# Kernel optimization log

Hardware: AMD Instinct MI355X
Metric: run time of the kernel (lower is better)

Reference implementation:

```python
import jax, jax.numpy as jnp
import numpy as np

D_MODEL = 512
NUM_HEADS = 8


def setup_inputs() -> dict:
    key = jax.random.key(0)
    ks = jax.random.split(key, 6)
    B, T, D = 4, 2048, D_MODEL
    x = jax.random.normal(ks[0], (B, T, D), dtype=jnp.float32)
    periods = jax.random.randint(ks[1], (B, NUM_HEADS), 0, 48)
    # nn.MultiheadAttention parameters: packed qkv in-projection + out-projection
    in_proj_w = jax.random.normal(ks[2], (3 * D, D), dtype=jnp.float32) * 0.02
    in_proj_b = jax.random.normal(ks[3], (3 * D,), dtype=jnp.float32) * 0.02
    out_w = jax.random.normal(ks[4], (D, D), dtype=jnp.float32) * 0.02
    out_b = jax.random.normal(ks[5], (D,), dtype=jnp.float32) * 0.02
    return {"x": x, "periods": periods, "in_proj_w": in_proj_w,
            "in_proj_b": in_proj_b, "out_w": out_w, "out_b": out_b}


def reference(x, periods, in_proj_w, in_proj_b, out_w, out_b):
    B, T, D = x.shape
    H = periods.shape[1]          # one head per period (num_heads == top_k)
    hd = D // H
    # packed qkv projection (matches torch in_proj_weight layout)
    qkv = x @ in_proj_w.T + in_proj_b            # (B,T,3D)
    q, k, v = jnp.split(qkv, 3, axis=-1)
    def to_heads(t):
        return t.reshape(B, T, H, hd).transpose(0, 2, 1, 3)  # (B,H,T,hd)
    q, k, v = to_heads(q), to_heads(k), to_heads(v)
    scores = jnp.einsum('bhqd,bhkd->bhqk', q, k) / jnp.sqrt(jnp.asarray(hd, x.dtype))
    # periodic causal mask: allow j<=i with (i-j) % P == 0
    i = jnp.arange(T)[:, None]
    j = jnp.arange(T)[None, :]
    p = jnp.maximum(periods, 1)[:, :, None, None]            # (B,H,1,1)
    allow = (j <= i) & (((i - j) % p) == 0)                  # (B,H,T,T)
    scores = jnp.where(allow, scores, -jnp.inf)              # diagonal always allowed -> no all-masked rows
    attn = jax.nn.softmax(scores, axis=-1)
    out = jnp.einsum('bhqk,bhkd->bhqd', attn, v)             # (B,H,T,hd)
    out = out.transpose(0, 2, 1, 3).reshape(B, T, D)
    return out @ out_w.T + out_b
```

## Files before the change

kernel.cpp:

```cpp
#include <hip/hip_runtime.h>
#include <math.h>

#define D_MODEL 512
#define NHEAD   8
#define HD      64
#define T_SEQ   2048
#define BATCH   4
#define M_ROWS  (BATCH * T_SEQ)

typedef __attribute__((ext_vector_type(8))) short  short8;
typedef __attribute__((ext_vector_type(4))) float  floatx4;

__device__ __forceinline__ unsigned short f2bf(float f) {
    unsigned int u = __float_as_uint(f);
    unsigned int r = u + 0x7FFFu + ((u >> 16) & 1u);
    return (unsigned short)(r >> 16);
}

__device__ __forceinline__ float bf2f(unsigned short u) {
    return __uint_as_float((unsigned int)u << 16);
}

__device__ __forceinline__ int4 cvt8(float4 a, float4 b) {
    union { unsigned short u[8]; int4 v; } r;
    r.u[0] = f2bf(a.x); r.u[1] = f2bf(a.y); r.u[2] = f2bf(a.z); r.u[3] = f2bf(a.w);
    r.u[4] = f2bf(b.x); r.u[5] = f2bf(b.y); r.u[6] = f2bf(b.z); r.u[7] = f2bf(b.w);
    return r.v;
}

__device__ __forceinline__ bool slot_decode(int t, int P, int& r, int& mt, int& Lr)
{
    const int q0 = T_SEQ / P, rem = T_SEQ % P;
    const int nt_hi = (q0 + 64) >> 6;
    const int nt_lo = (q0 + 63) >> 6;
    const int hi_total = rem * nt_hi;
    if (t < hi_total) {
        r = t / nt_hi; mt = t - r * nt_hi; Lr = q0 + 1;
    } else {
        t -= hi_total;
        if (t >= (P - rem) * nt_lo) return false;
        const int rr = t / nt_lo;
        r = rem + rr; mt = t - rr * nt_lo; Lr = q0;
    }
    return true;
}

__global__ __launch_bounds__(256) void qkv_gemm_mfma(
    const float* __restrict__ X,
    const float* __restrict__ W,
    const float* __restrict__ bias,
    unsigned short* __restrict__ qo, unsigned short* __restrict__ ko,
    unsigned short* __restrict__ vo)
{
    __shared__ unsigned short smem[128 * 128];
    unsigned short* const As = smem;
    unsigned short* const Bs = smem + 128 * 64;

    const int bid  = blockIdx.x;
    const int xcd  = bid & 7;
    const int chk_ = bid >> 3;
    const int row0 = (((chk_ / 12) << 3) + xcd) << 7;
    const int col0 = (chk_ % 12) << 7;

    const int tid  = threadIdx.x;
    const int wave = tid >> 6, lane = tid & 63;
    const int quad = lane >> 4, l15 = lane & 15;
    const int wm   = wave >> 1, wn = wave & 1;
    const int lr8  = lane >> 3;
    const int sc   = lane & 7;

    floatx4 acc[4][4] = {};

    for (int k0 = 0; k0 < D_MODEL; k0 += 64) {
        int4 av[4], bv[4];
#pragma unroll
        for (int i = 0; i < 4; ++i) {
            const int r = wave * 32 + i * 8 + lr8;
            const float* ap = X + (size_t)(row0 + r) * D_MODEL + k0 + (sc << 3);
            const float* bp = W + (size_t)(col0 + r) * D_MODEL + k0 + (sc << 3);
            av[i] = cvt8(*(const float4*)ap, *(const float4*)(ap + 4));
            bv[i] = cvt8(*(const float4*)bp, *(const float4*)(bp + 4));
        }
        __syncthreads();
#pragma unroll
        for (int i = 0; i < 4; ++i) {
            const int r  = wave * 32 + i * 8 + lr8;
            const int cp = (sc ^ (r & 7)) << 3;
            *(int4*)(As + (r << 6) + cp) = av[i];
            *(int4*)(Bs + (r << 6) + cp) = bv[i];
        }
        __syncthreads();

#pragma unroll
        for (int ks = 0; ks < 2; ++ks) {
            short8 af[4], bfr[4];
            const int ch = (ks << 2) + quad;
#pragma unroll
            for (int mt = 0; mt < 4; ++mt) {
                const int row = (wm << 6) + (mt << 4) + l15;
                af[mt] = *(const short8*)(As + (row << 6) + ((ch ^ (row & 7)) << 3));
            }
#pragma unroll
            for (int nt = 0; nt < 4; ++nt) {
                const int col = (wn << 6) + (nt << 4) + l15;
                bfr[nt] = *(const short8*)(Bs + (col << 6) + ((ch ^ (col & 7)) << 3));
            }
#pragma unroll
            for (int mt = 0; mt < 4; ++mt)
#pragma unroll
                for (int nt = 0; nt < 4; ++nt)
                    acc[mt][nt] = __builtin_amdgcn_mfma_f32_16x16x32_bf16(
                        af[mt], bfr[nt], acc[mt][nt], 0, 0, 0);
        }
    }

    __syncthreads();
#pragma unroll
    for (int nt = 0; nt < 4; ++nt) {
        const int ncol = (wn << 6) + (nt << 4) + l15;
        const float bn = bias[col0 + ncol];
#pragma unroll
        for (int mt = 0; mt < 4; ++mt)
#pragma unroll
            for (int reg = 0; reg < 4; ++reg) {
                const int mrow = (wm << 6) + (mt << 4) + (quad << 2) + reg;
                smem[(mrow << 7) + ncol] = f2bf(acc[mt][nt][reg] + bn);
            }
    }
    __syncthreads();
    {
        const int c16  = lane & 15;
        const int rsub = lane >> 4;
        const int n0   = col0 + (c16 << 3);
        const int part = n0 >> 9;
        unsigned short* dst = (part == 0) ? qo : ((part == 1) ? ko : vo);
        const int head = (n0 & 511) >> 6, d0 = n0 & 63;
#pragma unroll
        for (int p = 0; p < 8; ++p) {
            const int ml = (wave << 5) + (p << 2) + rsub;
            const int m  = row0 + ml;
            const int b = m >> 11, t = m & 2047;
            int4 val = *(const int4*)(smem + (ml << 7) + (c16 << 3));
            *(int4*)(dst + ((((size_t)b << 3) + head) * T_SEQ + t) * HD + d0) = val;
        }
    }
}

__global__ __launch_bounds__(256) void attn_rc_mfma(
    const unsigned short* __restrict__ q, const unsigned short* __restrict__ k,
    const unsigned short* __restrict__ v, const int* __restrict__ periods,
    unsigned short* __restrict__ o,
    unsigned short* __restrict__ Opart, float* __restrict__ Mpart,
    float* __restrict__ Lpart)
{
    __shared__ unsigned short Ks[2][64 * 64];
    __shared__ unsigned short Vt[2][64 * 64];
    __shared__ unsigned short Ps[64 * 64];

    const int bh = blockIdx.y;
    int P = periods[bh]; if (P < 1) P = 1;
    const int t_orig = blockIdx.x;
    const int c = blockIdx.z;
    int r, mt, Lr;
    if (!slot_decode(t_orig, P, r, mt, Lr)) return;
    if ((c << 3) > mt) return;
    const int nch  = (mt >> 3) + 1;
    const int kt0  = c << 3;
    const int kend = (kt0 + 7 < mt) ? (kt0 + 7) : mt;
    const int m0 = mt << 6;

    const int tid  = threadIdx.x;
    const int wave = tid >> 6, lane = tid & 63;
    const int quad = lane >> 4, l15 = lane & 15;
    const int srow = tid >> 2;
    const int vkp  = tid & 31, vhg = tid >> 5;

    const unsigned short* hq = q + (size_t)bh * T_SEQ * HD;
    const unsigned short* hk = k + (size_t)bh * T_SEQ * HD;
    const unsigned short* hv = v + (size_t)bh * T_SEQ * HD;

    const short8 vone = {16256, 16256, 16256, 16256,
                         16256, 16256, 16256, 16256};

    {
        int m = m0 + srow; if (m > Lr - 1) m = Lr - 1;
        const unsigned short* src = hq + (size_t)(r + m * P) * HD;
#pragma unroll
        for (int rep = 0; rep < 2; ++rep) {
            const int cc = ((tid & 3) << 1) + rep;
            int4 a = *(const int4*)(src + (cc << 3));
            *(int4*)(Ps + (srow << 6) + ((cc ^ (srow & 7)) << 3)) = a;
        }
    }
    {
        const int km0 = kt0 << 6;
        int mk = km0 + srow; if (mk > Lr - 1) mk = Lr - 1;
        const unsigned short* ksrc = hk + (size_t)(r + mk * P) * HD;
#pragma unroll
        for (int rep = 0; rep < 2; ++rep) {
            const int cc = ((tid & 3) << 1) + rep;
            int4 a = *(const int4*)(ksrc + (cc << 3));
            *(int4*)(Ks[0] + (srow << 6) + ((cc ^ (srow & 7)) << 3)) = a;
        }
        int mv0 = km0 + (vkp << 1);     if (mv0 > Lr - 1) mv0 = Lr - 1;
        int mv1 = km0 + (vkp << 1) + 1; if (mv1 > Lr - 1) mv1 = Lr - 1;
        int4 va = *(const int4*)(hv + (size_t)(r + mv0 * P) * HD + (vhg << 3));
        int4 vb = *(const int4*)(hv + (size_t)(r + mv1 * P) * HD + (vhg << 3));
        const unsigned short* pa = (const unsigned short*)&va;
        const unsigned short* pb = (const unsigned short*)&vb;
#pragma unroll
        for (int j = 0; j < 8; ++j) {
            const int hd_ = (vhg << 3) + j;
            const unsigned int pk =
                (unsigned int)pa[j] | ((unsigned int)pb[j] << 16);
            *(unsigned int*)((char*)Vt[0] + (hd_ << 7) +
                             ((((vkp >> 2) ^ (hd_ & 7)) << 4)) +
                             ((vkp & 3) << 2)) = pk;
        }
    }
    __syncthreads();
    short8 qf[2];
#pragma unroll
    for (int ks = 0; ks < 2; ++ks) {
        const int row = (wave << 4) + l15;
        qf[ks] = *(const short8*)(Ps + (row << 6) +
                                  ((((ks << 2) + quad) ^ (row & 7)) << 3));
    }

    floatx4 Oa[4] = {};
    float m_i[4] = {-1e30f, -1e30f, -1e30f, -1e30f};
    float l_i[4] = {0.f, 0.f, 0.f, 0.f};

    for (int kt = kt0; kt <= kend; ++kt) {
        const int buf = (kt - kt0) & 1;
        const bool havenext = kt < kend;

        int4 ka[2], va, vb;
        if (havenext) {
            const int km0 = (kt + 1) << 6;
            int mk = km0 + srow; if (mk > Lr - 1) mk = Lr - 1;
            const unsigned short* ksrc = hk + (size_t)(r + mk * P) * HD;
#pragma unroll
            for (int rep = 0; rep < 2; ++rep)
                ka[rep] = *(const int4*)(ksrc + ((((tid & 3) << 1) + rep) << 3));
            int mv0 = km0 + (vkp << 1);     if (mv0 > Lr - 1) mv0 = Lr - 1;
            int mv1 = km0 + (vkp << 1) + 1; if (mv1 > Lr - 1) mv1 = Lr - 1;
            va = *(const int4*)(hv + (size_t)(r + mv0 * P) * HD + (vhg << 3));
            vb = *(const int4*)(hv + (size_t)(r + mv1 * P) * HD + (vhg << 3));
        }

        floatx4 sacc[4] = {};
#pragma unroll
        for (int nt = 0; nt < 4; ++nt) {
            const int row = (nt << 4) + l15;
#pragma unroll
            for (int ks = 0; ks < 2; ++ks) {
                short8 kf = *(const short8*)(Ks[buf] + (row << 6) +
                                             ((((ks << 2) + quad) ^ (row & 7)) << 3));
                sacc[nt] = __builtin_amdgcn_mfma_f32_16x16x32_bf16(
                    qf[ks], kf, sacc[nt], 0, 0, 0);
            }
        }

        const bool diag = (kt == mt);
        float s[4][4];
        float tm = -1e30f;
#pragma unroll
        for (int nt = 0; nt < 4; ++nt)
#pragma unroll
            for (int reg = 0; reg < 4; ++reg) {
                float sv = sacc[nt][reg] * 0.125f;
                if (diag) {
                    const int sq = (wave << 4) + (quad << 2) + reg;
                    if (((nt << 4) + l15) > sq) sv = -1e30f;
                }
                s[nt][reg] = sv;
                tm = fmaxf(tm, sv);
            }
        tm = fmaxf(tm, __shfl_xor(tm, 1));
        tm = fmaxf(tm, __shfl_xor(tm, 2));
        tm = fmaxf(tm, __shfl_xor(tm, 4));
        tm = fmaxf(tm, __shfl_xor(tm, 8));
        tm = fmaxf(tm, __shfl_xor(tm, 16));
        tm = fmaxf(tm, __shfl_xor(tm, 32));

        float sc[4];
#pragma unroll
        for (int reg = 0; reg < 4; ++reg) {
            const float nm = fmaxf(m_i[reg], tm);
            sc[reg] = __expf(m_i[reg] - nm);
            m_i[reg] = nm;
        }

#pragma unroll
        for (int reg = 0; reg < 4; ++reg) {
            const int row = (wave << 4) + (quad << 2) + reg;
#pragma unroll
            for (int nt = 0; nt < 4; ++nt) {
                const int col = (nt << 4) + l15;
                *((unsigned short*)((char*)Ps + (row << 7) +
                                    (((col >> 3) ^ (row & 7)) << 4) +
                                    ((col & 7) << 1))) =
                    f2bf(__expf(s[nt][reg] - m_i[reg]));
            }
        }

        short8 pf[2];
#pragma unroll
        for (int ks = 0; ks < 2; ++ks) {
            const int row = (wave << 4) + l15;
            pf[ks] = *(const short8*)(Ps + (row << 6) +
                                      ((((ks << 2) + quad) ^ (row & 7)) << 3));
        }
        floatx4 ls = {};
        ls = __builtin_amdgcn_mfma_f32_16x16x32_bf16(pf[0], vone, ls, 0, 0, 0);
        ls = __builtin_amdgcn_mfma_f32_16x16x32_bf16(pf[1], vone, ls, 0, 0, 0);
#pragma unroll
        for (int reg = 0; reg < 4; ++reg)
            l_i[reg] = l_i[reg] * sc[reg] + ls[reg];

#pragma unroll
        for (int nt = 0; nt < 4; ++nt)
#pragma unroll
            for (int reg = 0; reg < 4; ++reg)
                Oa[nt][reg] *= sc[reg];
#pragma unroll
        for (int nt = 0; nt < 4; ++nt) {
            const int row = (nt << 4) + l15;
#pragma unroll
            for (int ks = 0; ks < 2; ++ks) {
                short8 vf = *(const short8*)(Vt[buf] + (row << 6) +
                                             ((((ks << 2) + quad) ^ (row & 7)) << 3));
                Oa[nt] = __builtin_amdgcn_mfma_f32_16x16x32_bf16(
                    pf[ks], vf, Oa[nt], 0, 0, 0);
            }
        }

        if (havenext) {
#pragma unroll
            for (int rep = 0; rep < 2; ++rep) {
                const int cc = ((tid & 3) << 1) + rep;
                *(int4*)(Ks[buf ^ 1] + (srow << 6) + ((cc ^ (srow & 7)) << 3)) = ka[rep];
            }
            const unsigned short* pa = (const unsigned short*)&va;
            const unsigned short* pb = (const unsigned short*)&vb;
#pragma unroll
            for (int j = 0; j < 8; ++j) {
                const int hd_ = (vhg << 3) + j;
                const unsigned int pk =
                    (unsigned int)pa[j] | ((unsigned int)pb[j] << 16);
                *(unsigned int*)((char*)Vt[buf ^ 1] + (hd_ << 7) +
                                 ((((vkp >> 2) ^ (hd_ & 7)) << 4)) +
                                 ((vkp & 3) << 2)) = pk;
            }
        }
        __syncthreads();
    }

    if (nch == 1) {
#pragma unroll
        for (int reg = 0; reg < 4; ++reg) {
            const float invl = 1.f / l_i[reg];
            const int row = (wave << 4) + (quad << 2) + reg;
#pragma unroll
            for (int nt = 0; nt < 4; ++nt)
                Ks[0][(row << 6) + (nt << 4) + l15] = f2bf(Oa[nt][reg] * invl);
        }
        const int lrow = lane >> 2;
        const int chk  = (lane & 3) << 1;
        const int ml   = (wave << 4) + lrow;
        const int m    = m0 + ml;
        if (m < Lr) {
            const size_t base = ((size_t)bh * T_SEQ + (r + m * P)) * HD;
            int4 w0 = *(const int4*)(Ks[0] + (ml << 6) + (chk << 3));
            int4 w1 = *(const int4*)(Ks[0] + (ml << 6) + ((chk + 1) << 3));
            *(int4*)(o + base + (chk << 3))       = w0;
            *(int4*)(o + base + ((chk + 1) << 3)) = w1;
        }
    } else {
        const size_t slot = ((size_t)((bh << 6) + t_orig) << 2) + c;
#pragma unroll
        for (int reg = 0; reg < 4; ++reg) {
            const int row = (wave << 4) + (quad << 2) + reg;
#pragma unroll
            for (int nt = 0; nt < 4; ++nt)
                Ks[0][(row << 6) + (nt << 4) + l15] = f2bf(Oa[nt][reg]);
            if (l15 == 0) {
                Mpart[slot * 64 + row] = m_i[reg];
                Lpart[slot * 64 + row] = l_i[reg];
            }
        }
        const int lrow = lane >> 2;
        const int chk  = (lane & 3) << 1;
        const int ml   = (wave << 4) + lrow;
        unsigned short* dst = Opart + slot * 4096 + (ml << 6);
        *(int4*)(dst + (chk << 3))       = *(const int4*)(Ks[0] + (ml << 6) + (chk << 3));
        *(int4*)(dst + ((chk + 1) << 3)) = *(const int4*)(Ks[0] + (ml << 6) + ((chk + 1) << 3));
    }
}

__global__ __launch_bounds__(256) void reduce_rc(
    const int* __restrict__ periods,
    const unsigned short* __restrict__ Opart, const float* __restrict__ Mpart,
    const float* __restrict__ Lpart, unsigned short* __restrict__ o)
{
    const int bh = blockIdx.y;
    int P = periods[bh]; if (P < 1) P = 1;
    const int t = blockIdx.x;
    int r, mt, Lr;
    if (!slot_decode(t, P, r, mt, Lr)) return;
    const int nch = (mt >> 3) + 1;
    if (nch < 2) return;

    const int tid = threadIdx.x;
    const int row = tid >> 2;
    const int cg  = (tid & 3) << 4;
    const int m   = (mt << 6) + row;
    if (m >= Lr) return;

    const size_t slot0 = (size_t)((bh << 6) + t) << 2;

    float mv[4], lv[4];
    float mm = -1e30f;
    for (int cc = 0; cc < nch; ++cc) {
        mv[cc] = Mpart[(slot0 + cc) * 64 + row];
        lv[cc] = Lpart[(slot0 + cc) * 64 + row];
        mm = fmaxf(mm, mv[cc]);
    }
    float lsum = 0.f, a[4];
    for (int cc = 0; cc < nch; ++cc) {
        a[cc] = __expf(mv[cc] - mm);
        lsum += a[cc] * lv[cc];
    }
    const float inv = 1.f / lsum;

    float ov[16] = {};
    for (int cc = 0; cc < nch; ++cc) {
        const unsigned short* p = Opart + (slot0 + cc) * 4096 + (row << 6) + cg;
        const float ac = a[cc];
#pragma unroll
        for (int j = 0; j < 16; ++j) ov[j] += ac * bf2f(p[j]);
    }
    unsigned short outv[16];
#pragma unroll
    for (int j = 0; j < 16; ++j) outv[j] = f2bf(ov[j] * inv);

    unsigned short* dst = o + ((size_t)bh * T_SEQ + (r + m * P)) * HD + cg;
    *(int4*)dst       = *(const int4*)&outv[0];
    *(int4*)(dst + 8) = *(const int4*)&outv[8];
}

__global__ __launch_bounds__(256) void out_gemm_mfma(
    const unsigned short* __restrict__ A,
    const float* __restrict__ W,
    const float* __restrict__ bias,
    float* __restrict__ out)
{
    __shared__ unsigned short As[128 * 64];
    __shared__ unsigned short Bs[128 * 64];

    const int tid  = threadIdx.x;
    const int wave = tid >> 6, lane = tid & 63;
    const int quad = lane >> 4, l15 = lane & 15;
    const int wm   = wave >> 1, wn = wave & 1;
    const int row0 = blockIdx.x * 128;
    const int col0 = blockIdx.y * 128;
    const int lr8  = lane >> 3;
    const int sc   = lane & 7;

    floatx4 acc[4][4] = {};

    for (int k0 = 0; k0 < D_MODEL; k0 += 64) {
        const int h = k0 >> 6;
        int4 av[4], bv[4];
#pragma unroll
        for (int i = 0; i < 4; ++i) {
            const int r  = wave * 32 + i * 8 + lr8;
            const int rg = row0 + r;
            const int b = rg >> 11, t = rg & 2047;
            av[i] = *(const int4*)(A + ((((size_t)b << 3) + h) * T_SEQ + t) * HD + (sc << 3));
            const float* bp = W + (size_t)(col0 + r) * D_MODEL + k0 + (sc << 3);
            bv[i] = cvt8(*(const float4*)bp, *(const float4*)(bp + 4));
        }
        __syncthreads();
#pragma unroll
        for (int i = 0; i < 4; ++i) {
            const int r  = wave * 32 + i * 8 + lr8;
            const int cp = (sc ^ (r & 7)) << 3;
            *(int4*)(As + (r << 6) + cp) = av[i];
            *(int4*)(Bs + (r << 6) + cp) = bv[i];
        }
        __syncthreads();

#pragma unroll
        for (int ks = 0; ks < 2; ++ks) {
            short8 af[4], bfr[4];
            const int ch = (ks << 2) + quad;
#pragma unroll
            for (int mt = 0; mt < 4; ++mt) {
                const int row = (wm << 6) + (mt << 4) + l15;
                af[mt] = *(const short8*)(As + (row << 6) + ((ch ^ (row & 7)) << 3));
            }
#pragma unroll
            for (int nt = 0; nt < 4; ++nt) {
                const int col = (wn << 6) + (nt << 4) + l15;
                bfr[nt] = *(const short8*)(Bs + (col << 6) + ((ch ^ (col & 7)) << 3));
            }
#pragma unroll
            for (int mt = 0; mt < 4; ++mt)
#pragma unroll
                for (int nt = 0; nt < 4; ++nt)
                    acc[mt][nt] = __builtin_amdgcn_mfma_f32_16x16x32_bf16(
                        af[mt], bfr[nt], acc[mt][nt], 0, 0, 0);
        }
    }

#pragma unroll
    for (int nt = 0; nt < 4; ++nt) {
        const int n = col0 + (wn << 6) + (nt << 4) + l15;
        const float bn = bias[n];
#pragma unroll
        for (int mt = 0; mt < 4; ++mt) {
#pragma unroll
            for (int reg = 0; reg < 4; ++reg) {
                const int m = row0 + (wm << 6) + (mt << 4) + (quad << 2) + reg;
                out[(size_t)m * D_MODEL + n] = acc[mt][nt][reg] + bn;
            }
        }
    }
}

extern "C" void kernel_launch(void* const* d_in, const int* in_sizes, int n_in,
                              void* d_out, int out_size, void* d_ws, size_t ws_size,
                              hipStream_t stream)
{
    const float* x        = (const float*)d_in[0];
    const int*   periods  = (const int*)  d_in[1];
    const float* in_w     = (const float*)d_in[2];
    const float* in_b     = (const float*)d_in[3];
    const float* out_w    = (const float*)d_in[4];
    const float* out_b    = (const float*)d_in[5];
    float*       out      = (float*)d_out;

    const size_t TENS = (size_t)BATCH * NHEAD * T_SEQ * HD;
    unsigned short* qb    = (unsigned short*)d_ws;
    unsigned short* kb    = qb + TENS;
    unsigned short* vb    = kb + TENS;
    unsigned short* aob   = vb + TENS;
    unsigned short* Opart = aob + TENS;
    float*          Mpart = (float*)(Opart + (size_t)8192 * 4096);
    float*          Lpart = Mpart + (size_t)8192 * 64;

    qkv_gemm_mfma<<<(M_ROWS / 128) * ((3 * D_MODEL) / 128), 256, 0, stream>>>(
        x, in_w, in_b, qb, kb, vb);

    dim3 g2(64, BATCH * NHEAD, 4);
    attn_rc_mfma<<<g2, 256, 0, stream>>>(qb, kb, vb, periods, aob,
                                         Opart, Mpart, Lpart);
    reduce_rc<<<dim3(64, BATCH * NHEAD), 256, 0, stream>>>(
        periods, Opart, Mpart, Lpart, aob);

    dim3 g3(M_ROWS / 128, D_MODEL / 128);
    out_gemm_mfma<<<g3, 256, 0, stream>>>(aob, out_w, out_b, out);
}
```

Baseline: 166.2 us.

## Pre-convert inputs to bf16 and stage GEMM tiles via direct global-to-LDS loads

Adds a conversion kernel that turns x and both weight matrices into bf16 buffers in workspace once per call. The QKV and output GEMMs then load these bf16 tiles straight into LDS with global_load_lds, using a swizzled source address instead of register staging, and add a barrier at the end of each k-step. The aim is to halve GEMM load bytes, stop each tile from re-converting the same weights, and skip the register round trip. The cost is an extra launch plus a full write and read of the bf16 copies.

```diff
diff --git a/kernel.cpp b/kernel.cpp
--- a/kernel.cpp
+++ b/kernel.cpp
@@ -26,6 +26,12 @@
     r.u[0] = f2bf(a.x); r.u[1] = f2bf(a.y); r.u[2] = f2bf(a.z); r.u[3] = f2bf(a.w);
     r.u[4] = f2bf(b.x); r.u[5] = f2bf(b.y); r.u[6] = f2bf(b.z); r.u[7] = f2bf(b.w);
     return r.v;
+}
+
+__device__ __forceinline__ void gload16(const void* g, void* l) {
+    __builtin_amdgcn_global_load_lds(
+        (const __attribute__((address_space(1))) void*)g,
+        (__attribute__((address_space(3))) void*)l, 16, 0, 0);
 }
 
 __device__ __forceinline__ bool slot_decode(int t, int P, int& r, int& mt, int& Lr)
@@ -45,9 +51,29 @@
     return true;
 }
 
+#define XGROUPS  (M_ROWS * D_MODEL / 8)
+#define W1GROUPS (3 * D_MODEL * D_MODEL / 8)
+#define W2GROUPS (D_MODEL * D_MODEL / 8)
+#define CVT_GROUPS (XGROUPS + W1GROUPS + W2GROUPS)
+
+__global__ __launch_bounds__(256) void cvt_inputs(
+    const float* __restrict__ x, const float* __restrict__ w1,
+    const float* __restrict__ w2, unsigned short* __restrict__ xo,
+    unsigned short* __restrict__ w1o, unsigned short* __restrict__ w2o)
+{
+    int i = blockIdx.x * 256 + threadIdx.x;
+    const float* src; unsigned short* dst;
+    if (i < XGROUPS)                  { src = x;  dst = xo;  }
+    else if (i < XGROUPS + W1GROUPS)  { src = w1; dst = w1o; i -= XGROUPS; }
+    else                              { src = w2; dst = w2o; i -= XGROUPS + W1GROUPS; }
+    const float4* p = (const float4*)(src + (size_t)i * 8);
+    float4 a = p[0], b = p[1];
+    *(int4*)(dst + (size_t)i * 8) = cvt8(a, b);
+}
+
 __global__ __launch_bounds__(256) void qkv_gemm_mfma(
-    const float* __restrict__ X,
-    const float* __restrict__ W,
+    const unsigned short* __restrict__ X,
+    const unsigned short* __restrict__ W,
     const float* __restrict__ bias,
     unsigned short* __restrict__ qo, unsigned short* __restrict__ ko,
     unsigned short* __restrict__ vo)
@@ -72,22 +98,15 @@
     floatx4 acc[4][4] = {};
 
     for (int k0 = 0; k0 < D_MODEL; k0 += 64) {
-        int4 av[4], bv[4];
 #pragma unroll
         for (int i = 0; i < 4; ++i) {
-            const int r = wave * 32 + i * 8 + lr8;
-            const float* ap = X + (size_t)(row0 + r) * D_MODEL + k0 + (sc << 3);
-            const float* bp = W + (size_t)(col0 + r) * D_MODEL + k0 + (sc << 3);
-            av[i] = cvt8(*(const float4*)ap, *(const float4*)(ap + 4));
-            bv[i] = cvt8(*(const float4*)bp, *(const float4*)(bp + 4));
-        }
-        __syncthreads();
-#pragma unroll
-        for (int i = 0; i < 4; ++i) {
-            const int r  = wave * 32 + i * 8 + lr8;
-            const int cp = (sc ^ (r & 7)) << 3;
-            *(int4*)(As + (r << 6) + cp) = av[i];
-            *(int4*)(Bs + (r << 6) + cp) = bv[i];
+            const int rb  = (wave << 5) + (i << 3);
+            const int r   = rb + lr8;
+            const int csw = sc ^ (r & 7);
+            gload16(X + (size_t)(row0 + r) * D_MODEL + k0 + (csw << 3),
+                    As + (rb << 6));
+            gload16(W + (size_t)(col0 + r) * D_MODEL + k0 + (csw << 3),
+                    Bs + (rb << 6));
         }
         __syncthreads();
 
@@ -112,9 +131,9 @@
                     acc[mt][nt] = __builtin_amdgcn_mfma_f32_16x16x32_bf16(
                         af[mt], bfr[nt], acc[mt][nt], 0, 0, 0);
         }
-    }
-
-    __syncthreads();
+        __syncthreads();
+    }
+
 #pragma unroll
     for (int nt = 0; nt < 4; ++nt) {
         const int ncol = (wn << 6) + (nt << 4) + l15;
@@ -452,7 +471,7 @@
 
 __global__ __launch_bounds__(256) void out_gemm_mfma(
     const unsigned short* __restrict__ A,
-    const float* __restrict__ W,
+    const unsigned short* __restrict__ W,
     const float* __restrict__ bias,
     float* __restrict__ out)
 {
@@ -472,23 +491,17 @@
 
     for (int k0 = 0; k0 < D_MODEL; k0 += 64) {
         const int h = k0 >> 6;
-        int4 av[4], bv[4];
 #pragma unroll
         for (int i = 0; i < 4; ++i) {
-            const int r  = wave * 32 + i * 8 + lr8;
+            const int rb  = (wave << 5) + (i << 3);
+            const int r   = rb + lr8;
+            const int csw = sc ^ (r & 7);
             const int rg = row0 + r;
             const int b = rg >> 11, t = rg & 2047;
-            av[i] = *(const int4*)(A + ((((size_t)b << 3) + h) * T_SEQ + t) * HD + (sc << 3));
-            const float* bp = W + (size_t)(col0 + r) * D_MODEL + k0 + (sc << 3);
-            bv[i] = cvt8(*(const float4*)bp, *(const float4*)(bp + 4));
-        }
-        __syncthreads();
-#pragma unroll
-        for (int i = 0; i < 4; ++i) {
-            const int r  = wave * 32 + i * 8 + lr8;
-            const int cp = (sc ^ (r & 7)) << 3;
-            *(int4*)(As + (r << 6) + cp) = av[i];
-            *(int4*)(Bs + (r << 6) + cp) = bv[i];
+            gload16(A + ((((size_t)b << 3) + h) * T_SEQ + t) * HD + (csw << 3),
+                    As + (rb << 6));
+            gload16(W + (size_t)(col0 + r) * D_MODEL + k0 + (csw << 3),
+                    Bs + (rb << 6));
         }
         __syncthreads();
 
@@ -513,6 +526,7 @@
                     acc[mt][nt] = __builtin_amdgcn_mfma_f32_16x16x32_bf16(
                         af[mt], bfr[nt], acc[mt][nt], 0, 0, 0);
         }
+        __syncthreads();
     }
 
 #pragma unroll
@@ -550,9 +564,14 @@
     unsigned short* Opart = aob + TENS;
     float*          Mpart = (float*)(Opart + (size_t)8192 * 4096);
     float*          Lpart = Mpart + (size_t)8192 * 64;
+    unsigned short* Xb    = (unsigned short*)(Lpart + (size_t)8192 * 64);
+    unsigned short* W1b   = Xb + (size_t)M_ROWS * D_MODEL;
+    unsigned short* W2b   = W1b + (size_t)3 * D_MODEL * D_MODEL;
+
+    cvt_inputs<<<CVT_GROUPS / 256, 256, 0, stream>>>(x, in_w, out_w, Xb, W1b, W2b);
 
     qkv_gemm_mfma<<<(M_ROWS / 128) * ((3 * D_MODEL) / 128), 256, 0, stream>>>(
-        x, in_w, in_b, qb, kb, vb);
+        Xb, W1b, in_b, qb, kb, vb);
 
     dim3 g2(64, BATCH * NHEAD, 4);
     attn_rc_mfma<<<g2, 256, 0, stream>>>(qb, kb, vb, periods, aob,
@@ -561,5 +580,5 @@
         periods, Opart, Mpart, Lpart, aob);
 
     dim3 g3(M_ROWS / 128, D_MODEL / 128);
-    out_gemm_mfma<<<g3, 256, 0, stream>>>(aob, out_w, out_b, out);
-}
+    out_gemm_mfma<<<g3, 256, 0, stream>>>(aob, W2b, out_b, out);
+}
```

After: 151.6 us. 1.1x faster.
